# Optimization experiments

Hardware: AMD Instinct MI355X
Metric: run time of the kernel (lower is better)

The kernel has to match this reference:

```python
import jax, jax.numpy as jnp
import numpy as np

# GGML Q8_0: each block = 2-byte fp16 scale + 32 int8 quants (gguf.GGML_QUANT_SIZES[Q8_0] = (32, 34))
BLOCK_SIZE = 32
TYPE_SIZE = 34
IN_FEATURES = 8192
OUT_FEATURES = 8192
BATCH = 16


def setup_inputs() -> dict:
    key = jax.random.key(0)
    kx, ks, kq, kb = jax.random.split(key, 4)
    x = jax.random.normal(kx, (BATCH, IN_FEATURES), dtype=jnp.float32)

    n_blocks = OUT_FEATURES * (IN_FEATURES // BLOCK_SIZE)
    # fp16 per-block scales, int8 quants, packed into the raw GGML byte layout
    scales = (jax.random.normal(ks, (n_blocks,), dtype=jnp.float32) * 0.01).astype(jnp.float16)
    quants = jax.random.randint(kq, (n_blocks, BLOCK_SIZE), -128, 128, dtype=jnp.int32).astype(jnp.int8)
    scale_bytes = np.asarray(scales).view(np.uint8).reshape(n_blocks, 2)  # little-endian fp16
    quant_bytes = np.asarray(quants).view(np.uint8)                       # [n_blocks, 32]
    raw = np.concatenate([scale_bytes, quant_bytes], axis=1).reshape(-1)  # [n_blocks * 34] uint8
    quantized_weight = jnp.asarray(raw)

    bias = jax.random.normal(kb, (OUT_FEATURES,), dtype=jnp.float32) * 0.01
    return {"x": x, "quantized_weight": quantized_weight, "bias": bias}


def dequantize_q8_0(raw, out_features, in_features):
    # raw: flat uint8 bytes in GGML Q8_0 layout -> [out_features, in_features] float32
    n_blocks = out_features * (in_features // BLOCK_SIZE)
    blk = raw.reshape(n_blocks, TYPE_SIZE)
    lo = blk[:, 0].astype(jnp.uint16)
    hi = blk[:, 1].astype(jnp.uint16)
    d = jax.lax.bitcast_convert_type(lo | (hi << 8), jnp.float16).astype(jnp.float32)  # [n_blocks]
    q = jax.lax.bitcast_convert_type(blk[:, 2:], jnp.int8).astype(jnp.float32)          # [n_blocks, 32]
    return (d[:, None] * q).reshape(out_features, in_features)


def reference(x, quantized_weight, bias):
    # tp_size == 1: column-parallel gather collective is the identity.
    w = dequantize_q8_0(quantized_weight, OUT_FEATURES, IN_FEATURES).astype(x.dtype)
    return x @ w.T + bias.astype(x.dtype)
```

## Files before the change

kernel.cpp:

```cpp
#include <hip/hip_runtime.h>
#include <stdint.h>


typedef _Float16 half8  __attribute__((ext_vector_type(8)));
typedef _Float16 half2v __attribute__((ext_vector_type(2)));
typedef float    float4v __attribute__((ext_vector_type(4)));
typedef uint32_t __attribute__((may_alias)) u32a;
typedef uint16_t __attribute__((may_alias)) u16a;
typedef uint4    __attribute__((may_alias)) u4a;
typedef float4v  __attribute__((may_alias)) f4a;

__device__ __forceinline__ uint32_t pack4(uint4 d) {
  uint32_t p01 = __builtin_amdgcn_perm(d.y, d.x, 0x0C0C0400u);
  uint32_t p23 = __builtin_amdgcn_perm(d.w, d.z, 0x04000C0Cu);
  return p01 | p23;
}

__device__ __forceinline__ uint32_t mpair(uint32_t t, uint32_t sel) {
  uint32_t d = __builtin_amdgcn_perm(t, 0x64646464u, sel);
  half2v v = __builtin_bit_cast(half2v, d);
  half2v m = __builtin_bit_cast(half2v, (uint32_t)0xE480E480u);
  v = v + m;
  return __builtin_bit_cast(uint32_t, v);
}

extern "C" __global__ __launch_bounds__(256, 2)
void q8lin_kernel(const float* __restrict__ x,
                  const int* __restrict__ wq,
                  const float* __restrict__ bias,
                  float* __restrict__ out)
{
  __shared__ __align__(16) unsigned char smem[4 * 8704];
  __shared__ __align__(16) float redbuf[4][16][16];

  const int tid  = threadIdx.x;
  const int wv   = tid >> 6;
  const int lane = tid & 63;
  const int c    = lane & 15;
  const int ksub = lane >> 4;
  const int g    = blockIdx.x;

  unsigned soff[5], wb[5];
#pragma unroll
  for (int r = 0; r < 5; ++r) {
    int u = r * 64 + lane; if (u > 271) u = 271;
    int cc = u / 17;
    int uu = u - cc * 17;
    soff[r] = (unsigned)(g * 16 + cc) * 8704u + (unsigned)uu * 16u;
    wb[r]   = (unsigned)u * 16u;
  }
  const unsigned kelem0 = (unsigned)wv * 2176u;
  unsigned char* buf0 = smem + wv * 8704;
  unsigned char* buf1 = buf0 + 4352;

  uint4 dg[20] = {};

  auto loadw = [&](int i) {
    const int* bp = wq + (kelem0 + (unsigned)i * 272u);
#pragma unroll
    for (int r = 0; r < 4; ++r)
#pragma unroll
      for (int s2 = 0; s2 < 4; ++s2)
        dg[r * 4 + s2] = *(const u4a*)(bp + soff[r] + s2 * 4);
    if (lane < 16) {
#pragma unroll
      for (int s2 = 0; s2 < 4; ++s2)
        dg[16 + s2] = *(const u4a*)(bp + soff[4] + s2 * 4);
    }
  };

  auto packwrite = [&](unsigned char* bufp) {
#pragma unroll
    for (int r = 0; r < 4; ++r) {
      uint4 pk;
      pk.x = pack4(dg[r * 4 + 0]); pk.y = pack4(dg[r * 4 + 1]);
      pk.z = pack4(dg[r * 4 + 2]); pk.w = pack4(dg[r * 4 + 3]);
      *(u4a*)(bufp + wb[r]) = pk;
    }
    if (lane < 16) {
      uint4 pk;
      pk.x = pack4(dg[16]); pk.y = pack4(dg[17]);
      pk.z = pack4(dg[18]); pk.w = pack4(dg[19]);
      *(u4a*)(bufp + wb[4]) = pk;
    }
  };

  float4v acc = {0.f, 0.f, 0.f, 0.f};

  auto process_chunk = [&](const unsigned char* bufc, int i) {
    const unsigned kabs0 = (unsigned)wv * 2048u + (unsigned)i * 256u;
#pragma unroll
    for (int j = 0; j < 8; ++j) {
      const unsigned blkoff = (unsigned)c * 272u + (unsigned)j * 34u;
      const unsigned short sb = *(const u16a*)(bufc + blkoff);
      const float dsc = (float)__builtin_bit_cast(_Float16, sb);
      uint32_t q0, q1, q2, q3;
      if ((j & 1) == 0) {
        const unsigned qo = blkoff + (unsigned)ksub * 8u;
        uint32_t d0 = *(const u32a*)(bufc + qo);
        uint32_t d1 = *(const u32a*)(bufc + qo + 4);
        uint32_t d2 = *(const u32a*)(bufc + qo + 8);
        d0 ^= 0x80808080u; d1 ^= 0x80808080u; d2 ^= 0x80808080u;
        q0 = mpair(d0, 0x00070006u);
        q1 = mpair(d1, 0x00050004u);
        q2 = mpair(d1, 0x00070006u);
        q3 = mpair(d2, 0x00050004u);
      } else {
        const unsigned qo = blkoff + 2u + (unsigned)ksub * 8u;
        uint32_t d0 = *(const u32a*)(bufc + qo);
        uint32_t d1 = *(const u32a*)(bufc + qo + 4);
        d0 ^= 0x80808080u; d1 ^= 0x80808080u;
        q0 = mpair(d0, 0x00050004u);
        q1 = mpair(d0, 0x00070006u);
        q2 = mpair(d1, 0x00050004u);
        q3 = mpair(d1, 0x00070006u);
      }
      half8 bfrag;
      { union { half8 h; uint32_t u[4]; } ub;
        ub.u[0] = q0; ub.u[1] = q1; ub.u[2] = q2; ub.u[3] = q3;
        bfrag = ub.h; }

      const unsigned kabs = kabs0 + (unsigned)j * 32u + (unsigned)ksub * 8u;
      const float* xp = x + (size_t)c * 8192 + kabs;
      float4v f0 = *(const f4a*)xp;
      float4v f1 = *(const f4a*)(xp + 4);
      half8 afrag;
      { union { half8 h; uint32_t u[4]; } ua;
        ua.u[0] = __builtin_bit_cast(uint32_t, __builtin_amdgcn_cvt_pkrtz(f0[0], f0[1]));
        ua.u[1] = __builtin_bit_cast(uint32_t, __builtin_amdgcn_cvt_pkrtz(f0[2], f0[3]));
        ua.u[2] = __builtin_bit_cast(uint32_t, __builtin_amdgcn_cvt_pkrtz(f1[0], f1[1]));
        ua.u[3] = __builtin_bit_cast(uint32_t, __builtin_amdgcn_cvt_pkrtz(f1[2], f1[3]));
        afrag = ua.h; }

      float4v D = __builtin_amdgcn_mfma_f32_16x16x32_f16(
          afrag, bfrag, (float4v){0.f, 0.f, 0.f, 0.f}, 0, 0, 0);
      acc[0] = fmaf(dsc, D[0], acc[0]);
      acc[1] = fmaf(dsc, D[1], acc[1]);
      acc[2] = fmaf(dsc, D[2], acc[2]);
      acc[3] = fmaf(dsc, D[3], acc[3]);
    }
  };

  loadw(0);
  packwrite(buf0);
#pragma unroll 1
  for (int i = 0; i < 7; ++i) {
    loadw(i + 1);
    process_chunk((i & 1) ? buf1 : buf0, i);
    packwrite(((i + 1) & 1) ? buf1 : buf0);
  }
  process_chunk(buf1, 7);

  *(f4a*)(&redbuf[wv][c][ksub * 4]) = acc;
  __syncthreads();
  {
    const int cc2 = tid & 15;
    const int rr  = tid >> 4;
    float s = redbuf[0][cc2][rr] + redbuf[1][cc2][rr]
            + redbuf[2][cc2][rr] + redbuf[3][cc2][rr]
            + bias[g * 16 + cc2];
    out[(size_t)rr * 8192 + (size_t)(g * 16 + cc2)] = s;
  }
}

extern "C" void kernel_launch(void* const* d_in, const int* in_sizes, int n_in,
                              void* d_out, int out_size, void* d_ws, size_t ws_size,
                              hipStream_t stream) {
  const float* x    = (const float*)d_in[0];
  const int*   wq   = (const int*)d_in[1];
  const float* bias = (const float*)d_in[2];
  float*       out  = (float*)d_out;
  (void)in_sizes; (void)n_in; (void)d_ws; (void)ws_size; (void)out_size;
  q8lin_kernel<<<dim3(8192 / 16), dim3(256), 0, stream>>>(x, wq, bias, out);
}
```

Baseline: 67.07 us.

## Drop LDS staging and read Q8_0 blocks directly from global with 8 waves

Removes the double-buffered shared-memory staging, where 16-byte loads were packed into bytes and then re-read. Each lane now loads its scale and quant words straight from global memory with 8-byte loads. A byte-pair permute plus magic-number trick turns the quants into fp16 MFMA operands. The block grows to 512 threads (8 waves, each covering 1024 K elements), with a final 8-way reduction in LDS. The aim is to cut LDS traffic and pack overhead and to lean on higher occupancy to hide latency. The cost is narrower global loads and no explicit software pipelining.

Measured after the change: 78.93 us. 1.18x slower.

```diff
diff --git a/kernel.cpp b/kernel.cpp
--- a/kernel.cpp
+++ b/kernel.cpp
@@ -2,36 +2,27 @@
 #include <stdint.h>
 
 
-typedef _Float16 half8  __attribute__((ext_vector_type(8)));
-typedef _Float16 half2v __attribute__((ext_vector_type(2)));
+typedef _Float16 half8   __attribute__((ext_vector_type(8)));
+typedef _Float16 half2v  __attribute__((ext_vector_type(2)));
 typedef float    float4v __attribute__((ext_vector_type(4)));
-typedef uint32_t __attribute__((may_alias)) u32a;
-typedef uint16_t __attribute__((may_alias)) u16a;
-typedef uint4    __attribute__((may_alias)) u4a;
+typedef uint2    __attribute__((may_alias)) u2a;
 typedef float4v  __attribute__((may_alias)) f4a;
 
-__device__ __forceinline__ uint32_t pack4(uint4 d) {
-  uint32_t p01 = __builtin_amdgcn_perm(d.y, d.x, 0x0C0C0400u);
-  uint32_t p23 = __builtin_amdgcn_perm(d.w, d.z, 0x04000C0Cu);
-  return p01 | p23;
-}
-
-__device__ __forceinline__ uint32_t mpair(uint32_t t, uint32_t sel) {
-  uint32_t d = __builtin_amdgcn_perm(t, 0x64646464u, sel);
-  half2v v = __builtin_bit_cast(half2v, d);
-  half2v m = __builtin_bit_cast(half2v, (uint32_t)0xE480E480u);
-  v = v + m;
+__device__ __forceinline__ uint32_t qpair(uint32_t lo, uint32_t hi) {
+  uint32_t r = __builtin_amdgcn_perm(hi, lo, 0x0C040C00u);
+  r ^= 0x64806480u;
+  half2v v = __builtin_bit_cast(half2v, r);
+  v = v + __builtin_bit_cast(half2v, (uint32_t)0xE480E480u);
   return __builtin_bit_cast(uint32_t, v);
 }
 
-extern "C" __global__ __launch_bounds__(256, 2)
+extern "C" __global__ __launch_bounds__(512, 4)
 void q8lin_kernel(const float* __restrict__ x,
                   const int* __restrict__ wq,
                   const float* __restrict__ bias,
                   float* __restrict__ out)
 {
-  __shared__ __align__(16) unsigned char smem[4 * 8704];
-  __shared__ __align__(16) float redbuf[4][16][16];
+  __shared__ __align__(16) float red[8][16][16];
 
   const int tid  = threadIdx.x;
   const int wv   = tid >> 6;
@@ -40,126 +31,61 @@
   const int ksub = lane >> 4;
   const int g    = blockIdx.x;
 
-  unsigned soff[5], wb[5];
-#pragma unroll
-  for (int r = 0; r < 5; ++r) {
-    int u = r * 64 + lane; if (u > 271) u = 271;
-    int cc = u / 17;
-    int uu = u - cc * 17;
-    soff[r] = (unsigned)(g * 16 + cc) * 8704u + (unsigned)uu * 16u;
-    wb[r]   = (unsigned)u * 16u;
-  }
-  const unsigned kelem0 = (unsigned)wv * 2176u;
-  unsigned char* buf0 = smem + wv * 8704;
-  unsigned char* buf1 = buf0 + 4352;
-
-  uint4 dg[20] = {};
-
-  auto loadw = [&](int i) {
-    const int* bp = wq + (kelem0 + (unsigned)i * 272u);
-#pragma unroll
-    for (int r = 0; r < 4; ++r)
-#pragma unroll
-      for (int s2 = 0; s2 < 4; ++s2)
-        dg[r * 4 + s2] = *(const u4a*)(bp + soff[r] + s2 * 4);
-    if (lane < 16) {
-#pragma unroll
-      for (int s2 = 0; s2 < 4; ++s2)
-        dg[16 + s2] = *(const u4a*)(bp + soff[4] + s2 * 4);
-    }
-  };
-
-  auto packwrite = [&](unsigned char* bufp) {
-#pragma unroll
-    for (int r = 0; r < 4; ++r) {
-      uint4 pk;
-      pk.x = pack4(dg[r * 4 + 0]); pk.y = pack4(dg[r * 4 + 1]);
-      pk.z = pack4(dg[r * 4 + 2]); pk.w = pack4(dg[r * 4 + 3]);
-      *(u4a*)(bufp + wb[r]) = pk;
-    }
-    if (lane < 16) {
-      uint4 pk;
-      pk.x = pack4(dg[16]); pk.y = pack4(dg[17]);
-      pk.z = pack4(dg[18]); pk.w = pack4(dg[19]);
-      *(u4a*)(bufp + wb[4]) = pk;
-    }
-  };
+  const int*   rowp = wq + (size_t)(g * 16 + c) * 8704 + (size_t)wv * 32 * 34;
+  const float* xrow = x + (size_t)c * 8192 + wv * 1024 + ksub * 8;
 
   float4v acc = {0.f, 0.f, 0.f, 0.f};
 
-  auto process_chunk = [&](const unsigned char* bufc, int i) {
-    const unsigned kabs0 = (unsigned)wv * 2048u + (unsigned)i * 256u;
+#pragma unroll 2
+  for (int j = 0; j < 32; ++j) {
+    const int* bp = rowp + j * 34;
+    u2a s01 = *(const u2a*)bp;
+    const int* qp = bp + 2 + ksub * 8;
+    u2a q0 = *(const u2a*)(qp + 0);
+    u2a q1 = *(const u2a*)(qp + 2);
+    u2a q2 = *(const u2a*)(qp + 4);
+    u2a q3 = *(const u2a*)(qp + 6);
+
+    uint32_t sv = __builtin_amdgcn_perm(s01.y, s01.x, 0x0C0C0400u);
+    const float dsc = (float)__builtin_bit_cast(_Float16, (uint16_t)sv);
+
+    half8 bfrag;
+    { union { half8 h; uint32_t u[4]; } ub;
+      ub.u[0] = qpair(q0.x, q0.y);
+      ub.u[1] = qpair(q1.x, q1.y);
+      ub.u[2] = qpair(q2.x, q2.y);
+      ub.u[3] = qpair(q3.x, q3.y);
+      bfrag = ub.h; }
+
+    const float* xp = xrow + j * 32;
+    float4v f0 = *(const f4a*)xp;
+    float4v f1 = *(const f4a*)(xp + 4);
+    half8 afrag;
+    { union { half8 h; uint32_t u[4]; } ua;
+      ua.u[0] = __builtin_bit_cast(uint32_t, __builtin_amdgcn_cvt_pkrtz(f0[0], f0[1]));
+      ua.u[1] = __builtin_bit_cast(uint32_t, __builtin_amdgcn_cvt_pkrtz(f0[2], f0[3]));
+      ua.u[2] = __builtin_bit_cast(uint32_t, __builtin_amdgcn_cvt_pkrtz(f1[0], f1[1]));
+      ua.u[3] = __builtin_bit_cast(uint32_t, __builtin_amdgcn_cvt_pkrtz(f1[2], f1[3]));
+      afrag = ua.h; }
+
+    float4v D = __builtin_amdgcn_mfma_f32_16x16x32_f16(
+        afrag, bfrag, (float4v){0.f, 0.f, 0.f, 0.f}, 0, 0, 0);
+    acc[0] = fmaf(dsc, D[0], acc[0]);
+    acc[1] = fmaf(dsc, D[1], acc[1]);
+    acc[2] = fmaf(dsc, D[2], acc[2]);
+    acc[3] = fmaf(dsc, D[3], acc[3]);
+  }
+
+  *(f4a*)(&red[wv][c][ksub * 4]) = acc;
+  __syncthreads();
+
+  if (tid < 256) {
+    const int cc = tid & 15;
+    const int rr = tid >> 4;
+    float s = bias[g * 16 + cc];
 #pragma unroll
-    for (int j = 0; j < 8; ++j) {
-      const unsigned blkoff = (unsigned)c * 272u + (unsigned)j * 34u;
-      const unsigned short sb = *(const u16a*)(bufc + blkoff);
-      const float dsc = (float)__builtin_bit_cast(_Float16, sb);
-      uint32_t q0, q1, q2, q3;
-      if ((j & 1) == 0) {
-        const unsigned qo = blkoff + (unsigned)ksub * 8u;
-        uint32_t d0 = *(const u32a*)(bufc + qo);
-        uint32_t d1 = *(const u32a*)(bufc + qo + 4);
-        uint32_t d2 = *(const u32a*)(bufc + qo + 8);
-        d0 ^= 0x80808080u; d1 ^= 0x80808080u; d2 ^= 0x80808080u;
-        q0 = mpair(d0, 0x00070006u);
-        q1 = mpair(d1, 0x00050004u);
-        q2 = mpair(d1, 0x00070006u);
-        q3 = mpair(d2, 0x00050004u);
-      } else {
-        const unsigned qo = blkoff + 2u + (unsigned)ksub * 8u;
-        uint32_t d0 = *(const u32a*)(bufc + qo);
-        uint32_t d1 = *(const u32a*)(bufc + qo + 4);
-        d0 ^= 0x80808080u; d1 ^= 0x80808080u;
-        q0 = mpair(d0, 0x00050004u);
-        q1 = mpair(d0, 0x00070006u);
-        q2 = mpair(d1, 0x00050004u);
-        q3 = mpair(d1, 0x00070006u);
-      }
-      half8 bfrag;
-      { union { half8 h; uint32_t u[4]; } ub;
-        ub.u[0] = q0; ub.u[1] = q1; ub.u[2] = q2; ub.u[3] = q3;
-        bfrag = ub.h; }
-
-      const unsigned kabs = kabs0 + (unsigned)j * 32u + (unsigned)ksub * 8u;
-      const float* xp = x + (size_t)c * 8192 + kabs;
-      float4v f0 = *(const f4a*)xp;
-      float4v f1 = *(const f4a*)(xp + 4);
-      half8 afrag;
-      { union { half8 h; uint32_t u[4]; } ua;
-        ua.u[0] = __builtin_bit_cast(uint32_t, __builtin_amdgcn_cvt_pkrtz(f0[0], f0[1]));
-        ua.u[1] = __builtin_bit_cast(uint32_t, __builtin_amdgcn_cvt_pkrtz(f0[2], f0[3]));
-        ua.u[2] = __builtin_bit_cast(uint32_t, __builtin_amdgcn_cvt_pkrtz(f1[0], f1[1]));
-        ua.u[3] = __builtin_bit_cast(uint32_t, __builtin_amdgcn_cvt_pkrtz(f1[2], f1[3]));
-        afrag = ua.h; }
-
-      float4v D = __builtin_amdgcn_mfma_f32_16x16x32_f16(
-          afrag, bfrag, (float4v){0.f, 0.f, 0.f, 0.f}, 0, 0, 0);
-      acc[0] = fmaf(dsc, D[0], acc[0]);
-      acc[1] = fmaf(dsc, D[1], acc[1]);
-      acc[2] = fmaf(dsc, D[2], acc[2]);
-      acc[3] = fmaf(dsc, D[3], acc[3]);
-    }
-  };
-
-  loadw(0);
-  packwrite(buf0);
-#pragma unroll 1
-  for (int i = 0; i < 7; ++i) {
-    loadw(i + 1);
-    process_chunk((i & 1) ? buf1 : buf0, i);
-    packwrite(((i + 1) & 1) ? buf1 : buf0);
-  }
-  process_chunk(buf1, 7);
-
-  *(f4a*)(&redbuf[wv][c][ksub * 4]) = acc;
-  __syncthreads();
-  {
-    const int cc2 = tid & 15;
-    const int rr  = tid >> 4;
-    float s = redbuf[0][cc2][rr] + redbuf[1][cc2][rr]
-            + redbuf[2][cc2][rr] + redbuf[3][cc2][rr]
-            + bias[g * 16 + cc2];
-    out[(size_t)rr * 8192 + (size_t)(g * 16 + cc2)] = s;
+    for (int w = 0; w < 8; ++w) s += red[w][cc][rr];
+    out[(size_t)rr * 8192 + (size_t)(g * 16 + cc)] = s;
   }
 }
 
@@ -171,5 +97,5 @@
   const float* bias = (const float*)d_in[2];
   float*       out  = (float*)d_out;
   (void)in_sizes; (void)n_in; (void)d_ws; (void)ws_size; (void)out_size;
-  q8lin_kernel<<<dim3(8192 / 16), dim3(256), 0, stream>>>(x, wq, bias, out);
+  q8lin_kernel<<<dim3(8192 / 16), dim3(512), 0, stream>>>(x, wq, bias, out);
 }
```
